# Performance work log

Measured on AMD Instinct MI355X. Metric: run time of the kernel, lower is better.

The kernel has to match this reference:

```python
import jax, jax.numpy as jnp
import numpy as np


def setup_inputs() -> dict:
    key = jax.random.key(0)
    k1, k2, k3, k4, k5 = jax.random.split(key, 5)
    B, C, H, W = 8, 512, 128, 128
    C2 = 128  # key_dim
    x = jax.random.normal(k1, (B, C, H, W), dtype=jnp.float32)
    # 1x1 conv weights stored as [out_ch, in_ch] (kernel is 1x1)
    wq = jax.random.normal(k2, (C2, C), dtype=jnp.float32) * (1.0 / np.sqrt(C))
    bq = jax.random.normal(k3, (C2,), dtype=jnp.float32) * 0.01
    wk = jax.random.normal(k4, (C2, C), dtype=jnp.float32) * (1.0 / np.sqrt(C))
    bk = jax.random.normal(k5, (C2,), dtype=jnp.float32) * 0.01
    return {"x": x, "wq": wq, "bq": bq, "wk": wk, "bk": bk}


def reference(x, wq, bq, wk, bk):
    # x: [B, C, H, W]
    # 1x1 conv projections (query_conv / key_conv)
    q = jnp.einsum('bchw,kc->bkhw', x, wq) + bq[None, :, None, None]  # [B,C2,H,W]
    k = jnp.einsum('bchw,kc->bkhw', x, wk) + bk[None, :, None, None]  # [B,C2,H,W]

    # --- attention along H axis (batched over W) ---
    # query_h = key.permute(0,3,2,1): [B,W,H,C2]; key_h = query.permute(0,3,1,2): [B,W,C2,H]
    energy_h = jnp.einsum('bwhc,bcgw->bwhg', jnp.transpose(k, (0, 3, 2, 1)), q)  # [B,W,H,H]
    attn_h = jax.nn.softmax(energy_h, axis=-1)
    # value_h = x.permute(0,3,2,1): [B,W,H,C]; out: [B,W,H,C] -> permute(0,3,2,1) -> [B,C,H,W]
    out_h = jnp.einsum('bwhg,bcgw->bchw', attn_h, x)

    # --- attention along W axis (batched over H) ---
    # query_w = key.permute(0,2,3,1): [B,H,W,C2]; key_w = query.permute(0,2,1,3): [B,H,C2,W]
    energy_w = jnp.einsum('bhwc,bchv->bhwv', jnp.transpose(k, (0, 2, 3, 1)), q)  # [B,H,W,W]
    attn_w = jax.nn.softmax(energy_w, axis=-1)
    # value_w = x.permute(0,2,3,1): [B,H,W,C]; out: [B,H,W,C] -> permute(0,3,1,2) -> [B,C,H,W]
    out_w = jnp.einsum('bhwv,bchv->bchw', attn_w, x)

    return out_h + out_w
```

## Files before the change

### kernel.cpp

```cpp
#include <hip/hip_runtime.h>
#include <hip/hip_fp16.h>

#define NB 8
#define NC 512
#define NK 128
#define NP 128
#define NHW 16384

typedef unsigned short u16;
typedef unsigned int u32;
typedef float f32x4 __attribute__((ext_vector_type(4)));
typedef _Float16 f16x8 __attribute__((ext_vector_type(8)));

__device__ __forceinline__ u16 f2h(float f) { return __half_as_ushort(__float2half(f)); }
__device__ __forceinline__ float h2f(u16 u) { return __half2float(__ushort_as_half(u)); }

__global__ __launch_bounds__(256) void wconv_kernel(const float* __restrict__ wq,
                                                    const float* __restrict__ wk,
                                                    u16* __restrict__ wh) {
    int row = blockIdx.x;
    const float* src = (row < 128) ? (wq + (size_t)row * NC) : (wk + (size_t)(row - 128) * NC);
    int t = threadIdx.x;
    float2 v = *(const float2*)(src + t * 2);
    ushort2 o; o.x = f2h(v.x); o.y = f2h(v.y);
    *(ushort2*)(wh + (size_t)row * NC + t * 2) = o;
}

__global__ __launch_bounds__(256) void convtr_kernel(const float* __restrict__ x,
                                                     u16* __restrict__ xt) {
    __shared__ u16 ts[32][36];
    int plane = blockIdx.y;
    int tile  = blockIdx.x;
    int h0 = (tile >> 2) * 32, w0 = (tile & 3) * 32;
    const float* ip = x + (size_t)plane * NHW;
    u16* op = xt + (size_t)plane * NHW;
    int r  = threadIdx.x >> 3;
    int c4 = (threadIdx.x & 7) * 4;
    float4 v = *(const float4*)(ip + (h0 + r) * NP + w0 + c4);
    ts[r][c4 + 0] = f2h(v.x); ts[r][c4 + 1] = f2h(v.y);
    ts[r][c4 + 2] = f2h(v.z); ts[r][c4 + 3] = f2h(v.w);
    __syncthreads();
    ushort4 o;
    o.x = ts[c4 + 0][r]; o.y = ts[c4 + 1][r]; o.z = ts[c4 + 2][r]; o.w = ts[c4 + 3][r];
    *(ushort4*)(op + (w0 + r) * NP + h0 + c4) = o;
}

#define XROW 40
__device__ __forceinline__ int xt2_off(int p, int cw) {
    int sw = ((p >> 3) & 3) << 2;
    return p * XROW + 2 * (cw ^ sw);
}

__global__ __launch_bounds__(256, 3) void proj_kernel(const float* __restrict__ x,
                                                      const u16* __restrict__ wh,
                                                      const float* __restrict__ bq,
                                                      const float* __restrict__ bk,
                                                      u16* __restrict__ q,
                                                      u16* __restrict__ k) {
    __shared__ __align__(16) u16 smem[9216];
    int b  = blockIdx.y;
    int p0 = blockIdx.x * 64;
    int tid = threadIdx.x;
    int lane = tid & 63, w = tid >> 6;
    int ln = lane & 15, g = lane >> 4;

    float biasv[4];
#pragma unroll
    for (int nf = 0; nf < 4; nf++) {
        int oc = w * 64 + nf * 16 + ln;
        biasv[nf] = (oc < 128) ? bq[oc] : bk[oc - 128];
    }

    f32x4 acc[4][4];
#pragma unroll
    for (int mf = 0; mf < 4; mf++)
#pragma unroll
        for (int nf = 0; nf < 4; nf++) acc[mf][nf] = 0.0f;

    int si  = tid >> 4;
    int spx = (tid & 15) * 4;

#define STAGE(buf, c0)                                                                  \
    {                                                                                   \
        const float* xa = x + ((size_t)(b * NC + (c0) + 2 * si)) * NHW + p0 + spx;      \
        const float* xb = xa + NHW;                                                     \
        float4 a0 = *(const float4*)xa;                                                 \
        float4 b0 = *(const float4*)xb;                                                 \
        float av[4] = {a0.x, a0.y, a0.z, a0.w};                                         \
        float bv[4] = {b0.x, b0.y, b0.z, b0.w};                                         \
        _Pragma("unroll") for (int j = 0; j < 4; j++) {                                 \
            ushort2 pk;                                                                 \
            pk.x = f2h(av[j]); pk.y = f2h(bv[j]);                                       \
            *(ushort2*)&smem[(buf) * 2560 + xt2_off(spx + j, si)] = pk;                 \
        }                                                                               \
    }

    STAGE(0, 0);
    __syncthreads();
    for (int t = 0; t < 16; ++t) {
        int c0 = t * 32;
        if (t < 15) STAGE((t + 1) & 1, c0 + 32);
        f16x8 bf[4];
#pragma unroll
        for (int nf = 0; nf < 4; nf++)
            bf[nf] = *(const f16x8*)&wh[((size_t)(w * 64 + nf * 16 + ln)) * NC + c0 + g * 8];
        f16x8 af[4];
#pragma unroll
        for (int mf = 0; mf < 4; mf++)
            af[mf] = *(const f16x8*)&smem[(t & 1) * 2560 + xt2_off(mf * 16 + ln, g * 4)];
#pragma unroll
        for (int mf = 0; mf < 4; mf++)
#pragma unroll
            for (int nf = 0; nf < 4; nf++)
                acc[mf][nf] = __builtin_amdgcn_mfma_f32_16x16x32_f16(af[mf], bf[nf], acc[mf][nf], 0, 0, 0);
        __syncthreads();
    }
#undef STAGE

#pragma unroll
    for (int pass = 0; pass < 2; pass++) {
        if ((w >> 1) == pass) {
            int colbase = (w & 1) * 64;
#pragma unroll
            for (int mf = 0; mf < 4; mf++)
#pragma unroll
                for (int nf = 0; nf < 4; nf++)
#pragma unroll
                    for (int rg = 0; rg < 4; rg++) {
                        int p = mf * 16 + g * 4 + rg;
                        smem[p * 136 + colbase + nf * 16 + ln] = f2h(acc[mf][nf][rg] + biasv[nf]);
                    }
        }
        __syncthreads();
        {
            int p = tid >> 2, seg = tid & 3;
            u16* dst = (pass == 0 ? q : k) + ((size_t)(b * NHW + p0 + p)) * NK + seg * 32;
            const u16* srcl = &smem[p * 136 + seg * 32];
            *(uint4*)(dst)     = *(const uint4*)(srcl);
            *(uint4*)(dst + 8) = *(const uint4*)(srcl + 8);
            *(uint4*)(dst + 16) = *(const uint4*)(srcl + 16);
            *(uint4*)(dst + 24) = *(const uint4*)(srcl + 24);
        }
        __syncthreads();
    }
}

template <int TR, int OH>
__global__ __launch_bounds__(256) void attn_kernel(const u16* __restrict__ q,
                                                   const u16* __restrict__ k,
                                                   const void* __restrict__ vsrc,
                                                   void* __restrict__ osrc) {
    __shared__ __align__(16) u16 smem[2 * 128 * 136];
    __shared__ float redmax[256];
    __shared__ float redsum[256];
    u16* Ks = smem;
    u16* Qs = smem + 128 * 136;
    u16* Al = smem;
    u16* Vl = smem + 128 * 136;

    int r = blockIdx.x, b = blockIdx.y;
    int tid = threadIdx.x;
    int lane = tid & 63, w = tid >> 6;
    int ln = lane & 15, g = lane >> 4;

    const size_t base = TR ? ((size_t)b * NHW + r) * NK : ((size_t)b * NHW + (size_t)r * NP) * NK;
    const int qrs = TR ? NP * NK : NK;

    {
        int j = tid >> 1, hf = tid & 1;
        const u16* qp2 = q + base + (size_t)j * qrs + hf * 64;
        const u16* kp2 = k + base + (size_t)j * qrs + hf * 64;
#pragma unroll
        for (int e = 0; e < 8; e++) {
            *(uint4*)&Qs[j * 136 + hf * 64 + e * 8] = *(const uint4*)(qp2 + e * 8);
            *(uint4*)&Ks[j * 136 + hf * 64 + e * 8] = *(const uint4*)(kp2 + e * 8);
        }
    }
    __syncthreads();

    int wj = w >> 1, wi = w & 1;
    f32x4 e[4][4];
#pragma unroll
    for (int mf = 0; mf < 4; mf++)
#pragma unroll
        for (int nf = 0; nf < 4; nf++) e[mf][nf] = 0.0f;
#pragma unroll
    for (int ks = 0; ks < 4; ks++) {
        f16x8 qa[4], kb[4];
#pragma unroll
        for (int mf = 0; mf < 4; mf++)
            qa[mf] = *(const f16x8*)&Qs[(wj * 64 + mf * 16 + ln) * 136 + ks * 32 + g * 8];
#pragma unroll
        for (int nf = 0; nf < 4; nf++)
            kb[nf] = *(const f16x8*)&Ks[(wi * 64 + nf * 16 + ln) * 136 + ks * 32 + g * 8];
#pragma unroll
        for (int mf = 0; mf < 4; mf++)
#pragma unroll
            for (int nf = 0; nf < 4; nf++)
                e[mf][nf] = __builtin_amdgcn_mfma_f32_16x16x32_f16(qa[mf], kb[nf], e[mf][nf], 0, 0, 0);
    }

    float pm[4];
#pragma unroll
    for (int nf = 0; nf < 4; nf++) {
        pm[nf] = -3.0e38f;
#pragma unroll
        for (int mf = 0; mf < 4; mf++)
#pragma unroll
            for (int rg = 0; rg < 4; rg++) pm[nf] = fmaxf(pm[nf], e[mf][nf][rg]);
        pm[nf] = fmaxf(pm[nf], __shfl_xor(pm[nf], 16));
        pm[nf] = fmaxf(pm[nf], __shfl_xor(pm[nf], 32));
    }
    if (g == 0) {
#pragma unroll
        for (int nf = 0; nf < 4; nf++) redmax[wj * 128 + wi * 64 + nf * 16 + ln] = pm[nf];
    }
    __syncthreads();
    float fm[4];
#pragma unroll
    for (int nf = 0; nf < 4; nf++) {
        int i = wi * 64 + nf * 16 + ln;
        fm[nf] = fmaxf(redmax[i], redmax[128 + i]);
    }
    float ps[4] = {0.f, 0.f, 0.f, 0.f};
#pragma unroll
    for (int mf = 0; mf < 4; mf++)
#pragma unroll
        for (int nf = 0; nf < 4; nf++)
#pragma unroll
            for (int rg = 0; rg < 4; rg++) {
                float v = __expf(e[mf][nf][rg] - fm[nf]);
                e[mf][nf][rg] = v;
                ps[nf] += v;
            }
#pragma unroll
    for (int nf = 0; nf < 4; nf++) {
        ps[nf] += __shfl_xor(ps[nf], 16);
        ps[nf] += __shfl_xor(ps[nf], 32);
    }
    if (g == 0) {
#pragma unroll
        for (int nf = 0; nf < 4; nf++) redsum[wj * 128 + wi * 64 + nf * 16 + ln] = ps[nf];
    }
    __syncthreads();
    float ivs[4];
#pragma unroll
    for (int nf = 0; nf < 4; nf++) {
        int i = wi * 64 + nf * 16 + ln;
        ivs[nf] = 1.0f / (redsum[i] + redsum[128 + i]);
    }
#pragma unroll
    for (int mf = 0; mf < 4; mf++)
#pragma unroll
        for (int nf = 0; nf < 4; nf++) {
            ushort4 pk;
            pk.x = f2h(e[mf][nf][0] * ivs[nf]);
            pk.y = f2h(e[mf][nf][1] * ivs[nf]);
            pk.z = f2h(e[mf][nf][2] * ivs[nf]);
            pk.w = f2h(e[mf][nf][3] * ivs[nf]);
            *(ushort4*)&Al[(wi * 64 + nf * 16 + ln) * 136 + wj * 64 + mf * 16 + g * 4] = pk;
        }
    __syncthreads();

    int wc = w >> 1, wi2 = w & 1;
    f16x8 bfr[4][4];
#pragma unroll
    for (int nf2 = 0; nf2 < 4; nf2++)
#pragma unroll
        for (int js = 0; js < 4; js++)
            bfr[nf2][js] = *(const f16x8*)&Al[(wi2 * 64 + nf2 * 16 + ln) * 136 + js * 32 + g * 8];

    int cc = tid >> 2, ch = (tid & 3) * 32;
    u16 vh[32];
#define LOADV(c0)                                                                           \
    {                                                                                       \
        if (TR == 0) {                                                                      \
            const float* vn = (const float*)vsrc + ((size_t)(b * NC + (c0) + cc)) * NHW +   \
                              (size_t)r * NP + ch;                                          \
            _Pragma("unroll") for (int e2 = 0; e2 < 8; e2++) {                              \
                float4 vv = *(const float4*)(vn + e2 * 4);                                  \
                vh[e2 * 4 + 0] = f2h(vv.x); vh[e2 * 4 + 1] = f2h(vv.y);                     \
                vh[e2 * 4 + 2] = f2h(vv.z); vh[e2 * 4 + 3] = f2h(vv.w);                     \
            }                                                                               \
        } else {                                                                            \
            const u16* vn = (const u16*)vsrc + ((size_t)(b * NC + (c0) + cc)) * NHW +       \
                            (size_t)r * NP + ch;                                            \
            _Pragma("unroll") for (int e2 = 0; e2 < 4; e2++)                                \
                *(uint4*)&vh[e2 * 8] = *(const uint4*)(vn + e2 * 8);                        \
        }                                                                                   \
    }

    LOADV(0);
    for (int c0 = 0; c0 < NC; c0 += 64) {
#pragma unroll
        for (int e2 = 0; e2 < 4; e2++)
            *(uint4*)&Vl[cc * 136 + ch + e2 * 8] = *(uint4*)&vh[e2 * 8];
        __syncthreads();
        if (c0 + 64 < NC) LOADV(c0 + 64);
        f32x4 o[2][4];
#pragma unroll
        for (int mf2 = 0; mf2 < 2; mf2++)
#pragma unroll
            for (int nf2 = 0; nf2 < 4; nf2++) o[mf2][nf2] = 0.0f;
#pragma unroll
        for (int js = 0; js < 4; js++) {
            f16x8 va[2];
#pragma unroll
            for (int mf2 = 0; mf2 < 2; mf2++)
                va[mf2] = *(const f16x8*)&Vl[(wc * 32 + mf2 * 16 + ln) * 136 + js * 32 + g * 8];
#pragma unroll
            for (int mf2 = 0; mf2 < 2; mf2++)
#pragma unroll
                for (int nf2 = 0; nf2 < 4; nf2++)
                    o[mf2][nf2] = __builtin_amdgcn_mfma_f32_16x16x32_f16(va[mf2], bfr[nf2][js], o[mf2][nf2], 0, 0, 0);
        }
#pragma unroll
        for (int mf2 = 0; mf2 < 2; mf2++)
#pragma unroll
            for (int nf2 = 0; nf2 < 4; nf2++)
#pragma unroll
                for (int rg = 0; rg < 4; rg++) {
                    int ci = c0 + wc * 32 + mf2 * 16 + g * 4 + rg;
                    int ii = wi2 * 64 + nf2 * 16 + ln;
                    size_t oa = ((size_t)(b * NC + ci)) * NHW + (size_t)r * NP + ii;
                    if (OH) ((u16*)osrc)[oa] = f2h(o[mf2][nf2][rg]);
                    else    ((float*)osrc)[oa] = o[mf2][nf2][rg];
                }
        __syncthreads();
    }
#undef LOADV
}

__global__ __launch_bounds__(256) void combine_kernel(const u16* __restrict__ owh,
                                                      const u16* __restrict__ oht,
                                                      float* __restrict__ out) {
    __shared__ u16 ts[32][36];
    int plane = blockIdx.y;
    int tile  = blockIdx.x;
    int h0 = (tile >> 2) * 32, w0 = (tile & 3) * 32;
    int r  = threadIdx.x >> 3;
    int c4 = (threadIdx.x & 7) * 4;
    ushort4 v = *(const ushort4*)(oht + (size_t)plane * NHW + (w0 + r) * NP + h0 + c4);
    ts[r][c4 + 0] = v.x; ts[r][c4 + 1] = v.y; ts[r][c4 + 2] = v.z; ts[r][c4 + 3] = v.w;
    __syncthreads();
    ushort4 a = *(const ushort4*)(owh + (size_t)plane * NHW + (h0 + r) * NP + w0 + c4);
    float4 o;
    o.x = h2f(a.x) + h2f(ts[c4 + 0][r]);
    o.y = h2f(a.y) + h2f(ts[c4 + 1][r]);
    o.z = h2f(a.z) + h2f(ts[c4 + 2][r]);
    o.w = h2f(a.w) + h2f(ts[c4 + 3][r]);
    *(float4*)(out + (size_t)plane * NHW + (h0 + r) * NP + w0 + c4) = o;
}

__global__ __launch_bounds__(256) void addtr_kernel(const u16* __restrict__ oht,
                                                    float* __restrict__ out) {
    __shared__ u16 ts[32][36];
    int plane = blockIdx.y;
    int tile  = blockIdx.x;
    int h0 = (tile >> 2) * 32, w0 = (tile & 3) * 32;
    int r  = threadIdx.x >> 3;
    int c4 = (threadIdx.x & 7) * 4;
    ushort4 v = *(const ushort4*)(oht + (size_t)plane * NHW + (w0 + r) * NP + h0 + c4);
    ts[r][c4 + 0] = v.x; ts[r][c4 + 1] = v.y; ts[r][c4 + 2] = v.z; ts[r][c4 + 3] = v.w;
    __syncthreads();
    float* dst = out + (size_t)plane * NHW + (h0 + r) * NP + w0 + c4;
    float4 cur = *(const float4*)dst;
    cur.x += h2f(ts[c4 + 0][r]);
    cur.y += h2f(ts[c4 + 1][r]);
    cur.z += h2f(ts[c4 + 2][r]);
    cur.w += h2f(ts[c4 + 3][r]);
    *(float4*)dst = cur;
}

extern "C" void kernel_launch(void* const* d_in, const int* in_sizes, int n_in,
                              void* d_out, int out_size, void* d_ws, size_t ws_size,
                              hipStream_t stream) {
    const float* x  = (const float*)d_in[0];
    const float* wq = (const float*)d_in[1];
    const float* bq = (const float*)d_in[2];
    const float* wk = (const float*)d_in[3];
    const float* bk = (const float*)d_in[4];
    float* out = (float*)d_out;

    const size_t QKE = (size_t)NB * NHW * NK;
    const size_t XE  = (size_t)NB * NC * NHW;
    const size_t WHE = (size_t)256 * 512;
    u16* wh  = (u16*)d_ws;
    u16* q   = wh + WHE;
    u16* k   = q + QKE;
    u16* xt  = k + QKE;
    u16* oht = xt + XE;
    u16* owh = oht + XE;
    const size_t need_big = (WHE + 2 * QKE + 3 * XE) * sizeof(u16);
    const bool big = ws_size >= need_big;

    dim3 blk(256);

    wconv_kernel<<<dim3(256), blk, 0, stream>>>(wq, wk, wh);
    convtr_kernel<<<dim3(16, NB * NC), blk, 0, stream>>>(x, xt);
    proj_kernel<<<dim3(NHW / 64, NB), blk, 0, stream>>>(x, wh, bq, bk, q, k);
    attn_kernel<1, 1><<<dim3(NP, NB), blk, 0, stream>>>(q, k, (const void*)xt, (void*)oht);
    if (big) {
        attn_kernel<0, 1><<<dim3(NP, NB), blk, 0, stream>>>(q, k, (const void*)x, (void*)owh);
        combine_kernel<<<dim3(16, NB * NC), blk, 0, stream>>>(owh, oht, out);
    } else {
        attn_kernel<0, 0><<<dim3(NP, NB), blk, 0, stream>>>(q, k, (const void*)x, (void*)out);
        addtr_kernel<<<dim3(16, NB * NC), blk, 0, stream>>>(oht, out);
    }
}
```

Measured before the change: 494.8 us.

## Halve attention LDS footprint via staged K halves and add fp16 copy of x

```diff
diff --git a/kernel.cpp b/kernel.cpp
--- a/kernel.cpp
+++ b/kernel.cpp
@@ -26,8 +26,10 @@
     *(ushort2*)(wh + (size_t)row * NC + t * 2) = o;
 }
 
+template <int XH>
 __global__ __launch_bounds__(256) void convtr_kernel(const float* __restrict__ x,
-                                                     u16* __restrict__ xt) {
+                                                     u16* __restrict__ xt,
+                                                     u16* __restrict__ xh) {
     __shared__ u16 ts[32][36];
     int plane = blockIdx.y;
     int tile  = blockIdx.x;
@@ -37,8 +39,11 @@
     int r  = threadIdx.x >> 3;
     int c4 = (threadIdx.x & 7) * 4;
     float4 v = *(const float4*)(ip + (h0 + r) * NP + w0 + c4);
-    ts[r][c4 + 0] = f2h(v.x); ts[r][c4 + 1] = f2h(v.y);
-    ts[r][c4 + 2] = f2h(v.z); ts[r][c4 + 3] = f2h(v.w);
+    ushort4 sh;
+    sh.x = f2h(v.x); sh.y = f2h(v.y); sh.z = f2h(v.z); sh.w = f2h(v.w);
+    if (XH) *(ushort4*)(xh + (size_t)plane * NHW + (h0 + r) * NP + w0 + c4) = sh;
+    ts[r][c4 + 0] = sh.x; ts[r][c4 + 1] = sh.y;
+    ts[r][c4 + 2] = sh.z; ts[r][c4 + 3] = sh.w;
     __syncthreads();
     ushort4 o;
     o.x = ts[c4 + 0][r]; o.y = ts[c4 + 1][r]; o.z = ts[c4 + 2][r]; o.w = ts[c4 + 3][r];
@@ -145,17 +150,17 @@
     }
 }
 
-template <int TR, int OH>
-__global__ __launch_bounds__(256) void attn_kernel(const u16* __restrict__ q,
-                                                   const u16* __restrict__ k,
-                                                   const void* __restrict__ vsrc,
-                                                   void* __restrict__ osrc) {
-    __shared__ __align__(16) u16 smem[2 * 128 * 136];
-    __shared__ float redmax[256];
-    __shared__ float redsum[256];
-    u16* Ks = smem;
-    u16* Qs = smem + 128 * 136;
+template <int TR, int OH, int VH>
+__global__ __launch_bounds__(256, 3) void attn_kernel(const u16* __restrict__ q,
+                                                      const u16* __restrict__ k,
+                                                      const void* __restrict__ vsrc,
+                                                      void* __restrict__ osrc) {
+    __shared__ __align__(16) u16 smem[128 * 136 + 64 * 136];
+    u16* Qs = smem;
     u16* Al = smem;
+    u16* KH = smem + 128 * 136;
+    float* redmax = (float*)(smem + 128 * 136);
+    float* redsum = redmax + 256;
     u16* Vl = smem + 128 * 136;
 
     int r = blockIdx.x, b = blockIdx.y;
@@ -169,12 +174,16 @@
     {
         int j = tid >> 1, hf = tid & 1;
         const u16* qp2 = q + base + (size_t)j * qrs + hf * 64;
-        const u16* kp2 = k + base + (size_t)j * qrs + hf * 64;
-#pragma unroll
-        for (int e = 0; e < 8; e++) {
-            *(uint4*)&Qs[j * 136 + hf * 64 + e * 8] = *(const uint4*)(qp2 + e * 8);
-            *(uint4*)&Ks[j * 136 + hf * 64 + e * 8] = *(const uint4*)(kp2 + e * 8);
-        }
+#pragma unroll
+        for (int e2 = 0; e2 < 8; e2++)
+            *(uint4*)&Qs[j * 136 + hf * 64 + e2 * 8] = *(const uint4*)(qp2 + e2 * 8);
+    }
+    {
+        int i = tid >> 2, seg = (tid & 3) * 32;
+        const u16* kp2 = k + base + (size_t)i * qrs + seg;
+#pragma unroll
+        for (int e2 = 0; e2 < 4; e2++)
+            *(uint4*)&KH[i * 136 + seg + e2 * 8] = *(const uint4*)(kp2 + e2 * 8);
     }
     __syncthreads();
 
@@ -184,21 +193,39 @@
     for (int mf = 0; mf < 4; mf++)
 #pragma unroll
         for (int nf = 0; nf < 4; nf++) e[mf][nf] = 0.0f;
-#pragma unroll
-    for (int ks = 0; ks < 4; ks++) {
-        f16x8 qa[4], kb[4];
-#pragma unroll
-        for (int mf = 0; mf < 4; mf++)
-            qa[mf] = *(const f16x8*)&Qs[(wj * 64 + mf * 16 + ln) * 136 + ks * 32 + g * 8];
-#pragma unroll
-        for (int nf = 0; nf < 4; nf++)
-            kb[nf] = *(const f16x8*)&Ks[(wi * 64 + nf * 16 + ln) * 136 + ks * 32 + g * 8];
-#pragma unroll
-        for (int mf = 0; mf < 4; mf++)
-#pragma unroll
-            for (int nf = 0; nf < 4; nf++)
-                e[mf][nf] = __builtin_amdgcn_mfma_f32_16x16x32_f16(qa[mf], kb[nf], e[mf][nf], 0, 0, 0);
-    }
+
+#pragma unroll
+    for (int hh = 0; hh < 2; hh++) {
+        if (hh == 1) {
+            __syncthreads();
+            int i = tid >> 2, seg = (tid & 3) * 32;
+            const u16* kp2 = k + base + (size_t)(64 + i) * qrs + seg;
+#pragma unroll
+            for (int e2 = 0; e2 < 4; e2++)
+                *(uint4*)&KH[i * 136 + seg + e2 * 8] = *(const uint4*)(kp2 + e2 * 8);
+            __syncthreads();
+        }
+#pragma unroll
+        for (int ks = 0; ks < 4; ks++) {
+            f16x8 qa[4], kb[2];
+#pragma unroll
+            for (int mf = 0; mf < 4; mf++)
+                qa[mf] = *(const f16x8*)&Qs[(wj * 64 + mf * 16 + ln) * 136 + ks * 32 + g * 8];
+#pragma unroll
+            for (int n16 = 0; n16 < 2; n16++)
+                kb[n16] = *(const f16x8*)&KH[(wi * 32 + n16 * 16 + ln) * 136 + ks * 32 + g * 8];
+#pragma unroll
+            for (int mf = 0; mf < 4; mf++)
+#pragma unroll
+                for (int n16 = 0; n16 < 2; n16++)
+                    e[mf][hh * 2 + n16] = __builtin_amdgcn_mfma_f32_16x16x32_f16(qa[mf], kb[n16], e[mf][hh * 2 + n16], 0, 0, 0);
+        }
+    }
+    __syncthreads();
+
+    int iof[4];
+#pragma unroll
+    for (int nf = 0; nf < 4; nf++) iof[nf] = (nf >> 1) * 64 + wi * 32 + (nf & 1) * 16 + ln;
 
     float pm[4];
 #pragma unroll
@@ -213,15 +240,13 @@
     }
     if (g == 0) {
 #pragma unroll
-        for (int nf = 0; nf < 4; nf++) redmax[wj * 128 + wi * 64 + nf * 16 + ln] = pm[nf];
+        for (int nf = 0; nf < 4; nf++) redmax[wj * 128 + iof[nf]] = pm[nf];
     }
     __syncthreads();
     float fm[4];
 #pragma unroll
-    for (int nf = 0; nf < 4; nf++) {
-        int i = wi * 64 + nf * 16 + ln;
-        fm[nf] = fmaxf(redmax[i], redmax[128 + i]);
-    }
+    for (int nf = 0; nf < 4; nf++)
+        fm[nf] = fmaxf(redmax[iof[nf]], redmax[128 + iof[nf]]);
     float ps[4] = {0.f, 0.f, 0.f, 0.f};
 #pragma unroll
     for (int mf = 0; mf < 4; mf++)
@@ -240,15 +265,13 @@
     }
     if (g == 0) {
 #pragma unroll
-        for (int nf = 0; nf < 4; nf++) redsum[wj * 128 + wi * 64 + nf * 16 + ln] = ps[nf];
+        for (int nf = 0; nf < 4; nf++) redsum[wj * 128 + iof[nf]] = ps[nf];
     }
     __syncthreads();
     float ivs[4];
 #pragma unroll
-    for (int nf = 0; nf < 4; nf++) {
-        int i = wi * 64 + nf * 16 + ln;
-        ivs[nf] = 1.0f / (redsum[i] + redsum[128 + i]);
-    }
+    for (int nf = 0; nf < 4; nf++)
+        ivs[nf] = 1.0f / (redsum[iof[nf]] + redsum[128 + iof[nf]]);
 #pragma unroll
     for (int mf = 0; mf < 4; mf++)
 #pragma unroll
@@ -258,7 +281,7 @@
             pk.y = f2h(e[mf][nf][1] * ivs[nf]);
             pk.z = f2h(e[mf][nf][2] * ivs[nf]);
             pk.w = f2h(e[mf][nf][3] * ivs[nf]);
-            *(ushort4*)&Al[(wi * 64 + nf * 16 + ln) * 136 + wj * 64 + mf * 16 + g * 4] = pk;
+            *(ushort4*)&Al[iof[nf] * 136 + wj * 64 + mf * 16 + g * 4] = pk;
         }
     __syncthreads();
 
@@ -274,7 +297,12 @@
     u16 vh[32];
 #define LOADV(c0)                                                                           \
     {                                                                                       \
-        if (TR == 0) {                                                                      \
+        if (VH) {                                                                           \
+            const u16* vn = (const u16*)vsrc + ((size_t)(b * NC + (c0) + cc)) * NHW +       \
+                            (size_t)r * NP + ch;                                            \
+            _Pragma("unroll") for (int e2 = 0; e2 < 4; e2++)                                \
+                *(uint4*)&vh[e2 * 8] = *(const uint4*)(vn + e2 * 8);                        \
+        } else {                                                                            \
             const float* vn = (const float*)vsrc + ((size_t)(b * NC + (c0) + cc)) * NHW +   \
                               (size_t)r * NP + ch;                                          \
             _Pragma("unroll") for (int e2 = 0; e2 < 8; e2++) {                              \
@@ -282,11 +310,6 @@
                 vh[e2 * 4 + 0] = f2h(vv.x); vh[e2 * 4 + 1] = f2h(vv.y);                     \
                 vh[e2 * 4 + 2] = f2h(vv.z); vh[e2 * 4 + 3] = f2h(vv.w);                     \
             }                                                                               \
-        } else {                                                                            \
-            const u16* vn = (const u16*)vsrc + ((size_t)(b * NC + (c0) + cc)) * NHW +       \
-                            (size_t)r * NP + ch;                                            \
-            _Pragma("unroll") for (int e2 = 0; e2 < 4; e2++)                                \
-                *(uint4*)&vh[e2 * 8] = *(const uint4*)(vn + e2 * 8);                        \
         }                                                                                   \
     }
 
@@ -391,20 +414,24 @@
     u16* xt  = k + QKE;
     u16* oht = xt + XE;
     u16* owh = oht + XE;
-    const size_t need_big = (WHE + 2 * QKE + 3 * XE) * sizeof(u16);
+    u16* xh  = owh + XE;
+    const size_t need_big = (WHE + 2 * QKE + 4 * XE) * sizeof(u16);
     const bool big = ws_size >= need_big;
 
     dim3 blk(256);
 
     wconv_kernel<<<dim3(256), blk, 0, stream>>>(wq, wk, wh);
-    convtr_kernel<<<dim3(16, NB * NC), blk, 0, stream>>>(x, xt);
     proj_kernel<<<dim3(NHW / 64, NB), blk, 0, stream>>>(x, wh, bq, bk, q, k);
-    attn_kernel<1, 1><<<dim3(NP, NB), blk, 0, stream>>>(q, k, (const void*)xt, (void*)oht);
+
     if (big) {
-        attn_kernel<0, 1><<<dim3(NP, NB), blk, 0, stream>>>(q, k, (const void*)x, (void*)owh);
+        convtr_kernel<1><<<dim3(16, NB * NC), blk, 0, stream>>>(x, xt, xh);
+        attn_kernel<1, 1, 1><<<dim3(NP, NB), blk, 0, stream>>>(q, k, (const void*)xt, (void*)oht);
+        attn_kernel<0, 1, 1><<<dim3(NP, NB), blk, 0, stream>>>(q, k, (const void*)xh, (void*)owh);
         combine_kernel<<<dim3(16, NB * NC), blk, 0, stream>>>(owh, oht, out);
     } else {
-        attn_kernel<0, 0><<<dim3(NP, NB), blk, 0, stream>>>(q, k, (const void*)x, (void*)out);
+        convtr_kernel<0><<<dim3(16, NB * NC), blk, 0, stream>>>(x, xt, (u16*)nullptr);
+        attn_kernel<1, 1, 1><<<dim3(NP, NB), blk, 0, stream>>>(q, k, (const void*)xt, (void*)oht);
+        attn_kernel<0, 0, 0><<<dim3(NP, NB), blk, 0, stream>>>(q, k, (const void*)x, (void*)out);
         addtr_kernel<<<dim3(16, NB * NC), blk, 0, stream>>>(oht, out);
     }
 }
```

New measurement: 536.5 us. 1.08x slower.
